# Performance work log

Measured on AMD Instinct MI355X. Metric: run time of the kernel, lower is better.

## Reference

```python
import jax, jax.numpy as jnp
import numpy as np

H, V, B, S = 2048, 32000, 16, 256

def setup_inputs() -> dict:
    key = jax.random.key(0)
    k1, k2, k3, k4 = jax.random.split(key, 4)
    # Parameters exactly as the torch __init__ builds them
    alpha_exp = jax.nn.softmax(jax.random.normal(k1, (H, H), dtype=jnp.float32), axis=1)   # transition probs [H,H]
    beta = jax.nn.log_softmax(jax.random.normal(k2, (H, V), dtype=jnp.float32), axis=1)    # emission log-probs [H,V]
    gamma = jax.nn.log_softmax(jax.random.normal(k3, (H,), dtype=jnp.float32), axis=0)     # initial-state logits [H]
    input_ids = jax.random.randint(k4, (B, S), 0, V)
    return {"input_ids": input_ids, "alpha_exp": alpha_exp, "beta": beta, "gamma": gamma}


def _hmm_forward(input_ids, alpha_exp, beta, gamma):
    # gamma stored as log-probs; forward re-softmaxes it (faithful to torch code)
    gamma_exp = jax.nn.softmax(gamma)                       # [H]
    ids = input_ids.T                                       # [S,B]
    mask = (ids != -1).astype(beta.dtype)                   # [S,B]; -1 = padding
    # input_probs[t,h,b] = beta[h, ids[t,b]] * mask
    ip = jnp.transpose(beta[:, ids], (1, 0, 2)) * mask[:, None, :]   # [S,H,B]
    ip_rev = ip[::-1]                                       # process t = S-1 .. 0

    def step(y, ipt):
        # log-domain backward recursion: y' = log(alpha_exp @ exp(y - ymax)) + ymax + emission
        ymax = jnp.max(y, axis=0, keepdims=True)            # [1,B]
        y = jnp.log(alpha_exp @ jnp.exp(y - ymax)) + ymax + ipt
        return y, y

    y0 = ip_rev[0]                                          # t = S-1: y starts at 0, += emission
    y_last, ys_rest = jax.lax.scan(step, y0, ip_rev[1:])
    ys = jnp.concatenate([y0[None], ys_rest], axis=0)       # [S,H,B], ys[i] is t = S-1-i

    ymax = jnp.max(y_last, axis=0)                          # [B]
    final = jnp.log(gamma_exp @ jnp.exp(y_last - ymax[None, :])) + ymax   # [B] per-seq loglik
    return ys, final


def reference(input_ids, alpha_exp, beta, gamma):
    return _hmm_forward(input_ids, alpha_exp, beta, gamma)
```

## Files before the change

### kernel.cpp

```cpp
#include <hip/hip_runtime.h>
#include <cstdint>
#include <cstddef>

#define Hh 2048
#define Vv 32000
#define Bb 16
#define Ss 256

typedef unsigned short ushort_t;
typedef unsigned int   uint_t;
typedef unsigned long long ull_t;

typedef __attribute__((ext_vector_type(8))) short short8;
typedef __attribute__((ext_vector_type(4))) float f32x4;

#define Z_SLOT   ((size_t)Bb * Hh * 2)
#define WS_NEED  ((size_t)3 * Z_SLOT)

#define LD_REL(p)     __hip_atomic_load((p), __ATOMIC_RELAXED, __HIP_MEMORY_SCOPE_AGENT)
#define ST_REL(p, v)  __hip_atomic_store((p), (v), __ATOMIC_RELAXED, __HIP_MEMORY_SCOPE_AGENT)

#define SGN64 0x8000800080008000ull
#define MAG64 0x7FFF7FFF7FFF7FFFull

__device__ __forceinline__ float b2f_u(uint_t u) {
  union { uint_t u; float f; } x; x.u = u; return x.f;
}
__device__ __forceinline__ ushort_t f2b(float f) {
  union { float f; uint_t u; } x; x.f = f;
  uint_t u = x.u;
  return (ushort_t)((u + 0x7FFFu + ((u >> 16) & 1u)) >> 16);
}
__device__ __forceinline__ uint_t umaxu(uint_t a, uint_t b) { return a > b ? a : b; }
__device__ __forceinline__ uint_t pkmax16(uint_t a, uint_t b) {
  uint_t lo = umaxu(a & 0xFFFFu, b & 0xFFFFu);
  uint_t hi = umaxu(a >> 16, b >> 16);
  return lo | (hi << 16);
}

__global__ __launch_bounds__(256, 1) void hmm_persist(
    const float* __restrict__ alpha,
    const float* __restrict__ beta,
    const int*  __restrict__ ids,
    const float* __restrict__ gamma,
    ushort_t* __restrict__ Zbuf,
    float* __restrict__ out)
{
  const int w    = blockIdx.x;
  const int g    = w & 7;
  const int wl   = w >> 3;
  const int c0   = g * 2;
  const int tid  = threadIdx.x;
  const int wv   = tid >> 6;
  const int lane = tid & 63;
  const int lrow = lane & 15;
  const int quad = lane >> 4;

  __shared__ __align__(16) ushort_t zTf[2 * 2080];
  __shared__ float ybuf[128];
  __shared__ float ipld[2][128];
  __shared__ uint_t redm[2][4];
  __shared__ __align__(16) float red[2][4][4][256];
  __shared__ float fred[4][4];
  __shared__ float mh2[2];

  ull_t* ZbA = (ull_t*)Zbuf;

  short8 afr[64];
  #pragma unroll
  for (int t = 0; t < 4; ++t) {
    #pragma unroll
    for (int kt = 0; kt < 16; ++kt) {
      const float* arow = alpha + (size_t)(wl * 64 + t * 16 + lrow) * Hh
                          + wv * 512 + kt * 32 + quad * 8;
      float4 f0 = *(const float4*)arow;
      float4 f1 = *(const float4*)(arow + 4);
      short8 fr;
      fr[0] = (short)f2b(f0.x); fr[1] = (short)f2b(f0.y);
      fr[2] = (short)f2b(f0.z); fr[3] = (short)f2b(f0.w);
      fr[4] = (short)f2b(f1.x); fr[5] = (short)f2b(f1.y);
      fr[6] = (short)f2b(f1.z); fr[7] = (short)f2b(f1.w);
      afr[t * 16 + kt] = fr;
    }
  }

  const int myc = tid & 1;
  const int myr = wl * 64 + (tid >> 1);
  float ipreg = 0.f;

  {
    if (tid < 128) {
      const int v = ids[(c0 + myc) * Ss + (Ss - 1)];
      float yv = beta[(size_t)myr * Vv + v];
      ybuf[tid] = yv;
      out[(size_t)myr * Bb + (c0 + myc)] = yv;
    }
    __syncthreads();
    if (tid < 32) {
      const int c = tid >> 4, q = tid & 15;
      uint_t b0 = f2b(__expf(ybuf[(q * 4 + 0) * 2 + c]));
      uint_t b1 = f2b(__expf(ybuf[(q * 4 + 1) * 2 + c]));
      uint_t b2 = f2b(__expf(ybuf[(q * 4 + 2) * 2 + c]));
      uint_t b3 = f2b(__expf(ybuf[(q * 4 + 3) * 2 + c]));
      ull_t val = (ull_t)(b0 | (b1 << 16)) | ((ull_t)(b2 | (b3 << 16)) << 32);
      ST_REL(ZbA + (size_t)(c0 + c) * 512 + (wl * 16 + q), val);
    }
    if (tid < 128) {
      const int v1 = ids[(c0 + myc) * Ss + (Ss - 2)];
      ipreg = beta[(size_t)myr * Vv + v1];
    }
    __syncthreads();
  }

  const int h4a = wv * 128 + lane;
  const int h4b = h4a + 64;
  const size_t go0 = (size_t)c0 * 512 + h4a;
  const size_t go1 = (size_t)c0 * 512 + h4b;
  const size_t go2 = (size_t)(c0 + 1) * 512 + h4a;
  const size_t go3 = (size_t)(c0 + 1) * 512 + h4b;

  float mprev = 0.f;
  const ushort_t* zbase = zTf + (lrow & 1) * 2080 + quad * 8;

  const int  ec  = lrow;
  const int  rb  = wl * 64 + wv * 16 + quad * 4;
  const bool act = (lrow < 2);
  float pendy[4] = {0.f, 0.f, 0.f, 0.f};

  for (int k = 1; k < Ss; ++k) {
    const int   pb    = k & 1;
    const int   physR = (3 - ((k - 1) % 3)) % 3;
    const ull_t expS  = ((k - 1) & 1) ? SGN64 : 0ull;
    const size_t sb   = (size_t)physR * 8192;

    ull_t z0 = LD_REL(ZbA + sb + go0), z1 = LD_REL(ZbA + sb + go1);
    ull_t z2 = LD_REL(ZbA + sb + go2), z3 = LD_REL(ZbA + sb + go3);
    while ((((z0 ^ expS) | (z1 ^ expS) | (z2 ^ expS) | (z3 ^ expS)) & SGN64) != 0ull) {
      if ((z0 & SGN64) != expS) z0 = LD_REL(ZbA + sb + go0);
      if ((z1 & SGN64) != expS) z1 = LD_REL(ZbA + sb + go1);
      if ((z2 & SGN64) != expS) z2 = LD_REL(ZbA + sb + go2);
      if ((z3 & SGN64) != expS) z3 = LD_REL(ZbA + sb + go3);
    }

    uint_t m0, m1;
    {
      const ull_t u0 = z0 & MAG64, u1 = z1 & MAG64;
      const ull_t u2 = z2 & MAG64, u3 = z3 & MAG64;
      *(ull_t*)(zTf + 4 * h4a)        = u0;
      *(ull_t*)(zTf + 4 * h4b)        = u1;
      *(ull_t*)(zTf + 2080 + 4 * h4a) = u2;
      *(ull_t*)(zTf + 2080 + 4 * h4b) = u3;
      uint_t t0 = pkmax16(pkmax16((uint_t)u0, (uint_t)(u0 >> 32)),
                          pkmax16((uint_t)u1, (uint_t)(u1 >> 32)));
      uint_t t1 = pkmax16(pkmax16((uint_t)u2, (uint_t)(u2 >> 32)),
                          pkmax16((uint_t)u3, (uint_t)(u3 >> 32)));
      m0 = umaxu(t0 & 0xFFFFu, t0 >> 16);
      m1 = umaxu(t1 & 0xFFFFu, t1 >> 16);
    }
    if (tid < 128) ipld[pb][tid] = ipreg;
    uint_t pk = m0 | (m1 << 16);
    #pragma unroll
    for (int d = 1; d < 64; d <<= 1)
      pk = pkmax16(pk, (uint_t)__shfl_xor((int)pk, d));
    if (lane == 0) redm[pb][wv] = pk;

    asm volatile("s_waitcnt lgkmcnt(0)" ::: "memory");
    __builtin_amdgcn_sched_barrier(0);

    if (k < Ss - 1 && tid < 128) {
      const int v = ids[(c0 + myc) * Ss + (Ss - 2 - k)];
      ipreg = beta[(size_t)myr * Vv + v];
    }

    f32x4 acc0 = {0.f, 0.f, 0.f, 0.f}, acc1 = acc0, acc2 = acc0, acc3 = acc0;
    #pragma unroll
    for (int kt = 0; kt < 16; ++kt) {
      short8 bfr = *(const short8*)(zbase + (wv * 16 + kt) * 32);
      acc0 = __builtin_amdgcn_mfma_f32_16x16x32_bf16(afr[kt],      bfr, acc0, 0, 0, 0);
      acc1 = __builtin_amdgcn_mfma_f32_16x16x32_bf16(afr[16 + kt], bfr, acc1, 0, 0, 0);
      acc2 = __builtin_amdgcn_mfma_f32_16x16x32_bf16(afr[32 + kt], bfr, acc2, 0, 0, 0);
      acc3 = __builtin_amdgcn_mfma_f32_16x16x32_bf16(afr[48 + kt], bfr, acc3, 0, 0, 0);
    }

    if (wv != 0) *(f32x4*)&red[pb][0][wv][lane * 4] = acc0;
    if (wv != 1) *(f32x4*)&red[pb][1][wv][lane * 4] = acc1;
    if (wv != 2) *(f32x4*)&red[pb][2][wv][lane * 4] = acc2;
    if (wv != 3) *(f32x4*)&red[pb][3][wv][lane * 4] = acc3;
    __syncthreads();
    f32x4 sf = acc0;
    if (wv == 1) sf = acc1;
    else if (wv == 2) sf = acc2;
    else if (wv == 3) sf = acc3;
    #pragma unroll
    for (int v = 0; v < 4; ++v)
      if (v != wv) sf += *(const f32x4*)&red[pb][wv][v][lane * 4];

    const uint_t rr = pkmax16(pkmax16(redm[pb][0], redm[pb][1]),
                              pkmax16(redm[pb][2], redm[pb][3]));
    const uint_t mm = (lrow & 1) ? (rr >> 16) : (rr & 0xFFFFu);
    const float lmax = __logf(b2f_u(mm << 16));
    float ipv[4];
    #pragma unroll
    for (int i = 0; i < 4; ++i)
      ipv[i] = ipld[pb][(wv * 16 + quad * 4 + i) * 2 + (lrow & 1)];

    const float mnew = mprev + lmax;
    if (act) {
      float yv4[4];
      #pragma unroll
      for (int i = 0; i < 4; ++i)
        yv4[i] = __logf(sf[i]) + mprev + ipv[i];
      uint_t o0 = (uint_t)f2b(__expf(yv4[0] - mnew)) |
                  ((uint_t)f2b(__expf(yv4[1] - mnew)) << 16);
      uint_t o1 = (uint_t)f2b(__expf(yv4[2] - mnew)) |
                  ((uint_t)f2b(__expf(yv4[3] - mnew)) << 16);
      const int   physW = (3 - (k % 3)) % 3;
      const ull_t orS   = (k & 1) ? SGN64 : 0ull;
      ST_REL(ZbA + (size_t)physW * 8192 + (size_t)(c0 + ec) * 512 + (rb >> 2),
             ((ull_t)o0 | ((ull_t)o1 << 32)) | orS);
      #pragma unroll
      for (int i = 0; i < 4; ++i)
        out[(size_t)(k - 1) * (Hh * Bb) + (size_t)(rb + i) * Bb + (c0 + ec)] = pendy[i];
      #pragma unroll
      for (int i = 0; i < 4; ++i) pendy[i] = yv4[i];
    }
    mprev = mnew;
  }

  if (act) {
    #pragma unroll
    for (int i = 0; i < 4; ++i)
      out[(size_t)(Ss - 1) * (Hh * Bb) + (size_t)(rb + i) * Bb + (c0 + ec)] = pendy[i];
  }

  if (wl == 0) {
    if (tid < 2) mh2[tid] = mprev;
    __syncthreads();
    float4 ga = *(const float4*)(gamma + wv * 512 + 4 * lane);
    float4 gb = *(const float4*)(gamma + wv * 512 + 256 + 4 * lane);
    float gmx = fmaxf(fmaxf(fmaxf(ga.x, ga.y), fmaxf(ga.z, ga.w)),
                      fmaxf(fmaxf(gb.x, gb.y), fmaxf(gb.z, gb.w)));
    #pragma unroll
    for (int d = 1; d < 64; d <<= 1) gmx = fmaxf(gmx, __shfl_xor(gmx, d));
    if (lane == 0) fred[wv][0] = gmx;
    __syncthreads();
    const float gm = fmaxf(fmaxf(fred[0][0], fred[1][0]),
                           fmaxf(fred[2][0], fred[3][0]));
    float wga[4], wgb[4];
    wga[0] = __expf(ga.x - gm); wga[1] = __expf(ga.y - gm);
    wga[2] = __expf(ga.z - gm); wga[3] = __expf(ga.w - gm);
    wgb[0] = __expf(gb.x - gm); wgb[1] = __expf(gb.y - gm);
    wgb[2] = __expf(gb.z - gm); wgb[3] = __expf(gb.w - gm);
    float s1 = ((wga[0] + wga[1]) + (wga[2] + wga[3])) +
               ((wgb[0] + wgb[1]) + (wgb[2] + wgb[3]));
    ull_t z0 = LD_REL(ZbA + go0), z1 = LD_REL(ZbA + go1);
    ull_t z2 = LD_REL(ZbA + go2), z3 = LD_REL(ZbA + go3);
    while ((((z0 ^ SGN64) | (z1 ^ SGN64) | (z2 ^ SGN64) | (z3 ^ SGN64)) & SGN64) != 0ull) {
      if ((z0 & SGN64) != SGN64) z0 = LD_REL(ZbA + go0);
      if ((z1 & SGN64) != SGN64) z1 = LD_REL(ZbA + go1);
      if ((z2 & SGN64) != SGN64) z2 = LD_REL(ZbA + go2);
      if ((z3 & SGN64) != SGN64) z3 = LD_REL(ZbA + go3);
    }
    float s2a = 0.f, s2b = 0.f;
    #pragma unroll
    for (int i = 0; i < 4; ++i) {
      s2a += wga[i] * b2f_u(((uint_t)(z0 >> (16 * i)) & 0x7FFFu) << 16);
      s2a += wgb[i] * b2f_u(((uint_t)(z1 >> (16 * i)) & 0x7FFFu) << 16);
      s2b += wga[i] * b2f_u(((uint_t)(z2 >> (16 * i)) & 0x7FFFu) << 16);
      s2b += wgb[i] * b2f_u(((uint_t)(z3 >> (16 * i)) & 0x7FFFu) << 16);
    }
    #pragma unroll
    for (int d = 1; d < 64; d <<= 1) {
      s1  += __shfl_xor(s1, d);
      s2a += __shfl_xor(s2a, d);
      s2b += __shfl_xor(s2b, d);
    }
    if (lane == 0) { fred[wv][1] = s1; fred[wv][2] = s2a; fred[wv][3] = s2b; }
    __syncthreads();
    if (tid == 0) {
      float S1 = ((fred[0][1] + fred[1][1]) + (fred[2][1] + fred[3][1]));
      float Sa = ((fred[0][2] + fred[1][2]) + (fred[2][2] + fred[3][2]));
      float Sb = ((fred[0][3] + fred[1][3]) + (fred[2][3] + fred[3][3]));
      const float ls1 = __logf(S1);
      out[(size_t)Ss * Hh * Bb + c0]     = __logf(Sa) - ls1 + mh2[0];
      out[(size_t)Ss * Hh * Bb + c0 + 1] = __logf(Sb) - ls1 + mh2[1];
    }
  }
}

extern "C" void kernel_launch(void* const* d_in, const int* in_sizes, int n_in,
                              void* d_out, int out_size, void* d_ws, size_t ws_size,
                              hipStream_t stream) {
  (void)in_sizes; (void)n_in; (void)out_size;
  const int*   ids   = (const int*)d_in[0];
  const float* alpha = (const float*)d_in[1];
  const float* beta  = (const float*)d_in[2];
  const float* gamma = (const float*)d_in[3];
  float* out = (float*)d_out;
  char* ws = (char*)d_ws;

  if (ws_size < WS_NEED) return;

  ushort_t* Zbuf = (ushort_t*)ws;

  hipMemsetAsync(ws, 0x80, 2 * Z_SLOT, stream);
  hipMemsetAsync(ws + 2 * Z_SLOT, 0x00, Z_SLOT, stream);

  {
    const float* a_alpha = alpha;
    const float* a_beta  = beta;
    const int*   a_ids   = ids;
    const float* a_gamma = gamma;
    ushort_t* a_z = Zbuf;  float* a_out = out;
    void* args[] = {(void*)&a_alpha, (void*)&a_beta, (void*)&a_ids,
                    (void*)&a_gamma, (void*)&a_z, (void*)&a_out};
    hipError_t e = hipLaunchCooperativeKernel((const void*)hmm_persist,
                                              dim3(256), dim3(256), args, 0, stream);
    if (e != hipSuccess) {
      hipLaunchKernelGGL(hmm_persist, dim3(256), dim3(256), 0, stream,
                         alpha, beta, ids, gamma, Zbuf, out);
    }
  }
}
```

Measured before the change: 1.726 ms.

## Poll inter-block flags with wide coherent loads, backoff, and early emission prefetch

Each lane now owns two adjacent 64-bit slots, so the per-step flag polling becomes two 128-bit global loads with sc0 sc1 (cache-bypassing) in inline asm. Polling sleeps briefly after failed attempts, and the LDS stores and gamma indexing are updated to the new lane-to-slot mapping. The next step's emission gather (ids→beta) is issued before the spin-wait, so its latency overlaps the wait. The intent is fewer memory transactions per poll, less polling traffic between blocks, and hidden gather latency. The risk is that s_sleep adds latency on the serial critical path, and a torn 128-bit read is handled only by re-polling.

Result: faster. 1.473 ms (-14.6%).

```diff
diff --git a/kernel.cpp b/kernel.cpp
--- a/kernel.cpp
+++ b/kernel.cpp
@@ -13,6 +13,7 @@
 
 typedef __attribute__((ext_vector_type(8))) short short8;
 typedef __attribute__((ext_vector_type(4))) float f32x4;
+typedef __attribute__((ext_vector_type(2))) ull_t ullx2;
 
 #define Z_SLOT   ((size_t)Bb * Hh * 2)
 #define WS_NEED  ((size_t)3 * Z_SLOT)
@@ -112,12 +113,9 @@
     __syncthreads();
   }
 
-  const int h4a = wv * 128 + lane;
-  const int h4b = h4a + 64;
-  const size_t go0 = (size_t)c0 * 512 + h4a;
-  const size_t go1 = (size_t)c0 * 512 + h4b;
-  const size_t go2 = (size_t)(c0 + 1) * 512 + h4a;
-  const size_t go3 = (size_t)(c0 + 1) * 512 + h4b;
+  const int hp  = wv * 128 + 2 * lane;
+  const size_t go0 = (size_t)c0 * 512 + hp;
+  const size_t go2 = (size_t)(c0 + 1) * 512 + hp;
 
   float mprev = 0.f;
   const ushort_t* zbase = zTf + (lrow & 1) * 2080 + quad * 8;
@@ -133,23 +131,43 @@
     const ull_t expS  = ((k - 1) & 1) ? SGN64 : 0ull;
     const size_t sb   = (size_t)physR * 8192;
 
-    ull_t z0 = LD_REL(ZbA + sb + go0), z1 = LD_REL(ZbA + sb + go1);
-    ull_t z2 = LD_REL(ZbA + sb + go2), z3 = LD_REL(ZbA + sb + go3);
-    while ((((z0 ^ expS) | (z1 ^ expS) | (z2 ^ expS) | (z3 ^ expS)) & SGN64) != 0ull) {
-      if ((z0 & SGN64) != expS) z0 = LD_REL(ZbA + sb + go0);
-      if ((z1 & SGN64) != expS) z1 = LD_REL(ZbA + sb + go1);
-      if ((z2 & SGN64) != expS) z2 = LD_REL(ZbA + sb + go2);
-      if ((z3 & SGN64) != expS) z3 = LD_REL(ZbA + sb + go3);
+    float ipnext = 0.f;
+    if (k < Ss - 1 && tid < 128) {
+      const int v = ids[(c0 + myc) * Ss + (Ss - 2 - k)];
+      ipnext = beta[(size_t)myr * Vv + v];
+    }
+
+    ull_t z0, z1, z2, z3;
+    {
+      const ull_t* a01 = (const ull_t*)(ZbA + sb + go0);
+      const ull_t* a23 = (const ull_t*)(ZbA + sb + go2);
+      int r = 0;
+      for (;;) {
+        ullx2 pA, pB;
+        asm volatile(
+          "global_load_dwordx4 %0, %2, off sc0 sc1\n\t"
+          "global_load_dwordx4 %1, %3, off sc0 sc1\n\t"
+          "s_waitcnt vmcnt(0)"
+          : "=&v"(pA), "=&v"(pB)
+          : "v"(a01), "v"(a23)
+          : "memory");
+        z0 = pA.x; z1 = pA.y; z2 = pB.x; z3 = pB.y;
+        if ((((z0 ^ expS) | (z1 ^ expS) | (z2 ^ expS) | (z3 ^ expS)) & SGN64) == 0ull)
+          break;
+        if (r >= 3)      __builtin_amdgcn_s_sleep(16);
+        else if (r >= 1) __builtin_amdgcn_s_sleep(4);
+        ++r;
+      }
     }
 
     uint_t m0, m1;
     {
       const ull_t u0 = z0 & MAG64, u1 = z1 & MAG64;
       const ull_t u2 = z2 & MAG64, u3 = z3 & MAG64;
-      *(ull_t*)(zTf + 4 * h4a)        = u0;
-      *(ull_t*)(zTf + 4 * h4b)        = u1;
-      *(ull_t*)(zTf + 2080 + 4 * h4a) = u2;
-      *(ull_t*)(zTf + 2080 + 4 * h4b) = u3;
+      ullx2 w0; w0.x = u0; w0.y = u1;
+      ullx2 w1; w1.x = u2; w1.y = u3;
+      *(ullx2*)(zTf + wv * 512 + 8 * lane)        = w0;
+      *(ullx2*)(zTf + 2080 + wv * 512 + 8 * lane) = w1;
       uint_t t0 = pkmax16(pkmax16((uint_t)u0, (uint_t)(u0 >> 32)),
                           pkmax16((uint_t)u1, (uint_t)(u1 >> 32)));
       uint_t t1 = pkmax16(pkmax16((uint_t)u2, (uint_t)(u2 >> 32)),
@@ -158,6 +176,7 @@
       m1 = umaxu(t1 & 0xFFFFu, t1 >> 16);
     }
     if (tid < 128) ipld[pb][tid] = ipreg;
+    ipreg = ipnext;
     uint_t pk = m0 | (m1 << 16);
     #pragma unroll
     for (int d = 1; d < 64; d <<= 1)
@@ -166,11 +185,6 @@
 
     asm volatile("s_waitcnt lgkmcnt(0)" ::: "memory");
     __builtin_amdgcn_sched_barrier(0);
-
-    if (k < Ss - 1 && tid < 128) {
-      const int v = ids[(c0 + myc) * Ss + (Ss - 2 - k)];
-      ipreg = beta[(size_t)myr * Vv + v];
-    }
 
     f32x4 acc0 = {0.f, 0.f, 0.f, 0.f}, acc1 = acc0, acc2 = acc0, acc3 = acc0;
     #pragma unroll
@@ -236,8 +250,8 @@
   if (wl == 0) {
     if (tid < 2) mh2[tid] = mprev;
     __syncthreads();
-    float4 ga = *(const float4*)(gamma + wv * 512 + 4 * lane);
-    float4 gb = *(const float4*)(gamma + wv * 512 + 256 + 4 * lane);
+    float4 ga = *(const float4*)(gamma + wv * 512 + 8 * lane);
+    float4 gb = *(const float4*)(gamma + wv * 512 + 8 * lane + 4);
     float gmx = fmaxf(fmaxf(fmaxf(ga.x, ga.y), fmaxf(ga.z, ga.w)),
                       fmaxf(fmaxf(gb.x, gb.y), fmaxf(gb.z, gb.w)));
     #pragma unroll
@@ -253,13 +267,13 @@
     wgb[2] = __expf(gb.z - gm); wgb[3] = __expf(gb.w - gm);
     float s1 = ((wga[0] + wga[1]) + (wga[2] + wga[3])) +
                ((wgb[0] + wgb[1]) + (wgb[2] + wgb[3]));
-    ull_t z0 = LD_REL(ZbA + go0), z1 = LD_REL(ZbA + go1);
-    ull_t z2 = LD_REL(ZbA + go2), z3 = LD_REL(ZbA + go3);
+    ull_t z0 = LD_REL(ZbA + go0), z1 = LD_REL(ZbA + go0 + 1);
+    ull_t z2 = LD_REL(ZbA + go2), z3 = LD_REL(ZbA + go2 + 1);
     while ((((z0 ^ SGN64) | (z1 ^ SGN64) | (z2 ^ SGN64) | (z3 ^ SGN64)) & SGN64) != 0ull) {
       if ((z0 & SGN64) != SGN64) z0 = LD_REL(ZbA + go0);
-      if ((z1 & SGN64) != SGN64) z1 = LD_REL(ZbA + go1);
+      if ((z1 & SGN64) != SGN64) z1 = LD_REL(ZbA + go0 + 1);
       if ((z2 & SGN64) != SGN64) z2 = LD_REL(ZbA + go2);
-      if ((z3 & SGN64) != SGN64) z3 = LD_REL(ZbA + go3);
+      if ((z3 & SGN64) != SGN64) z3 = LD_REL(ZbA + go2 + 1);
     }
     float s2a = 0.f, s2b = 0.f;
     #pragma unroll
```
